# Kernel tuning notes

Hardware: AMD Instinct MI355X
Metric: run time of the kernel (lower is better)

## Reference

```python
import jax, jax.numpy as jnp
import numpy as np

B, S, H = 4, 512, 128

def setup_inputs() -> dict:
    key = jax.random.key(0)
    k_inp, k_m, k_w0, k_b0, k_w1, k_b1 = jax.random.split(key, 6)
    inp = jax.random.normal(k_inp, (B, S, H), dtype=jnp.float32)
    masks = jax.random.randint(k_m, (B, S), 0, 2, dtype=jnp.int32)
    # nn.Linear params: weight [out,in], bias [out]
    lim = 1.0 / np.sqrt(H)
    W0 = jax.random.uniform(k_w0, (H, H), jnp.float32, -lim, lim)
    b0 = jax.random.uniform(k_b0, (H,), jnp.float32, -lim, lim)
    W1 = jax.random.uniform(k_w1, (H, H), jnp.float32, -lim, lim)
    b1 = jax.random.uniform(k_b1, (H,), jnp.float32, -lim, lim)
    return {"inp": inp, "masks": masks, "W0": W0, "b0": b0, "W1": W1, "b1": b1}

def reference(inp, masks, W0, b0, W1, b1):
    # inp: [B,S,H], masks: [B,S] int {0,1}
    mf = masks.astype(inp.dtype)
    sentence_lengths = jnp.sum(mf, axis=1)                      # [B]
    gate_0 = jnp.einsum('bsh,oh->bso', inp, W0) + b0            # [B,S,H]
    gate_1 = jnp.einsum('bsh,oh->bso', inp, W1) + b1            # [B,S,H]
    # pairwise broadcast gate: [B,S(i),S(j),H]
    forget_gate = jax.nn.sigmoid(gate_0[:, :, None, :] + gate_1[:, None, :, :])
    # gate the row-expanded input (inp indexed by j)
    forget_result = inp[:, None, :, :] * forget_gate            # [B,S,S,H]
    pair_mask = mf[:, :, None] * mf[:, None, :]                 # [B,S,S]
    context_sumup = jnp.sum(forget_result * pair_mask[:, :, :, None], axis=2)  # [B,S,H]
    context_vector = context_sumup / sentence_lengths[:, None, None]
    return jnp.tanh(context_vector)
```

## Files before the change

### kernel.cpp

```cpp
#include <hip/hip_runtime.h>
#include <hip/hip_bf16.h>


#define BB 4
#define SS 512
#define HH 128
#define RA 8
#define L2E 1.44269504088896f

__global__ __launch_bounds__(256) void kA(const float* __restrict__ inp,
                                          const int* __restrict__ masks,
                                          const float* __restrict__ W0,
                                          const float* __restrict__ b0,
                                          const float* __restrict__ W1,
                                          const float* __restrict__ b1,
                                          float* __restrict__ E0,
                                          float2* __restrict__ XE,
                                          int* __restrict__ valid_idx,
                                          int* __restrict__ nvalid,
                                          float* __restrict__ rcpL,
                                          float* __restrict__ out) {
    const int bid = blockIdx.x;
    if (bid == 512) {
        int wave = threadIdx.x >> 6, lane = threadIdx.x & 63;
        if (wave >= BB) return;
        int b = wave, base = 0;
        for (int c = 0; c < SS; c += 64) {
            int m = masks[b * SS + c + lane];
            unsigned long long bits = __ballot(m != 0);
            int pos = __popcll(bits & ((1ull << lane) - 1ull));
            if (m) valid_idx[b * SS + base + pos] = c + lane;
            base += __popcll(bits);
        }
        if (lane == 0) {
            nvalid[b] = base;
            rcpL[b] = base ? 1.0f / (float)base : 0.0f;
        }
        return;
    }

    __shared__ float4 sW[32 * 128];

    const int g = bid & 1;
    const int row0 = (bid >> 1) * RA;
    const float* __restrict__ W = g ? W1 : W0;

#pragma unroll
    for (int it = 0; it < 16; ++it) {
        const int flat = it * 256 + threadIdx.x;
        const int q = flat & 31;
        const int o = flat >> 5;
        const float4 w = *(const float4*)(W + (size_t)o * HH + q * 4);
        sW[q * 128 + (o ^ q)] = w;
    }
    __syncthreads();

    const int o = threadIdx.x & 127;
    const int rh = threadIdx.x >> 7;
    const int r0 = row0 + rh * 4;
    const float* __restrict__ xb = inp + (size_t)r0 * HH;
    const float bias = g ? b1[o] : b0[o];

    float acc[4] = {bias, bias, bias, bias};
#pragma unroll 4
    for (int q = 0; q < 32; ++q) {
        const float4 w = sW[q * 128 + (o ^ q)];
#pragma unroll
        for (int r = 0; r < 4; ++r) {
            const float4 x = *(const float4*)(xb + (size_t)r * HH + q * 4);
            float a = acc[r];
            a = fmaf(x.x, w.x, a);
            a = fmaf(x.y, w.y, a);
            a = fmaf(x.z, w.z, a);
            a = fmaf(x.w, w.w, a);
            acc[r] = a;
        }
    }

    if (g == 0) {
#pragma unroll
        for (int r = 0; r < 4; ++r)
            E0[(size_t)(r0 + r) * HH + o] = __builtin_amdgcn_exp2f(acc[r] * L2E);
#pragma unroll
        for (int r = 0; r < 4; ++r)
            if (masks[r0 + r] == 0) out[(size_t)(r0 + r) * HH + o] = 0.0f;
    } else {
#pragma unroll
        for (int r = 0; r < 4; ++r) {
            const float re1 = __builtin_amdgcn_exp2f(-acc[r] * L2E);
            const float x = inp[(size_t)(r0 + r) * HH + o];
            XE[(size_t)(r0 + r) * HH + o] = make_float2(x, re1);
        }
    }
}

__global__ __launch_bounds__(1024) void kB(const float* __restrict__ E0,
                                           const float2* __restrict__ XE,
                                           const int* __restrict__ valid_idx,
                                           const int* __restrict__ nvalid,
                                           const float* __restrict__ rcpL,
                                           float* __restrict__ out) {
    const int b = blockIdx.x >> 7;
    const int qi = blockIdx.x & 127;
    const int nv = nvalid[b];
    const int p0 = qi * 4;
    if (p0 >= nv) return;

    __shared__ float red[8][4][HH];
    __shared__ int s_vj[SS];

    const int tid = threadIdx.x;
    const int h = tid & 127;
    const int oc = tid >> 7;

    if (tid < nv) s_vj[tid] = valid_idx[b * SS + tid];
    __syncthreads();

    const size_t boff = (size_t)b * SS * HH;
    const float* __restrict__ E0b = E0 + boff;
    const float2* __restrict__ XEb = XE + boff;

    float e0r[4];
#pragma unroll
    for (int r = 0; r < 4; ++r)
        e0r[r] = (p0 + r < nv) ? E0b[(size_t)s_vj[p0 + r] * HH + h] : 0.0f;

    const int chunk = (nv + 7) >> 3;
    const int jb = oc * chunk;
    const int je = min(nv, jb + chunk);

    float acc[4] = {0.f, 0.f, 0.f, 0.f};
    float sumx = 0.f;
#pragma unroll 8
    for (int t = jb; t < je; ++t) {
        const int j = s_vj[t];
        const float2 v = XEb[(size_t)j * HH + h];
        const float x = v.x, re1 = v.y;
        sumx += x;
        const float xr = x * re1;
#pragma unroll
        for (int r = 0; r < 4; ++r)
            acc[r] = fmaf(xr, __builtin_amdgcn_rcpf(re1 + e0r[r]), acc[r]);
    }

#pragma unroll
    for (int r = 0; r < 4; ++r) red[oc][r][h] = sumx - acc[r];
    __syncthreads();

    if (tid < 512) {
        const int r = tid >> 7;
        if (p0 + r < nv) {
            const int hh = tid & 127;
            float s = 0.f;
#pragma unroll
            for (int q = 0; q < 8; ++q) s += red[q][r][hh];
            float x = s * rcpL[b];
            x = fminf(fmaxf(x, -30.0f), 30.0f);
            const float e = __builtin_amdgcn_exp2f(x * 2.885390081777927f);
            const float th = (e - 1.0f) * __builtin_amdgcn_rcpf(e + 1.0f);
            out[boff + (size_t)s_vj[p0 + r] * HH + hh] = th;
        }
    }
}

extern "C" void kernel_launch(void* const* d_in, const int* in_sizes, int n_in,
                              void* d_out, int out_size, void* d_ws, size_t ws_size,
                              hipStream_t stream) {
    const float* inp = (const float*)d_in[0];
    const int* masks = (const int*)d_in[1];
    const float* W0 = (const float*)d_in[2];
    const float* b0 = (const float*)d_in[3];
    const float* W1 = (const float*)d_in[4];
    const float* b1 = (const float*)d_in[5];
    float* out = (float*)d_out;

    const size_t nBSH = (size_t)BB * SS * HH;
    float* E0 = (float*)d_ws;
    float2* XE = (float2*)(E0 + nBSH);
    int* valid_idx = (int*)(XE + nBSH);
    int* nvalid = valid_idx + BB * SS;
    float* rcpL = (float*)(nvalid + BB);

    kA<<<513, 256, 0, stream>>>(inp, masks, W0, b0, W1, b1,
                                E0, XE, valid_idx, nvalid, rcpL, out);
    kB<<<BB * (SS / 4), 1024, 0, stream>>>(E0, XE, valid_idx, nvalid, rcpL, out);
}
```

Before: 30.64 us.

## Retile gate GEMM over output-column groups and reformulate sigmoid sum

The projection kernel now has each block own 8 output columns for 128 rows. It stages 32-row input tiles in padded shared memory and keeps a small weight slice resident, instead of loading the full weight matrix per block and reading inputs from global memory. The pairwise kernel computes x*t/(1+t) with t=e0*e1 directly, replacing the sumx minus x/(1+e0/e1) form. This drops the running sum and the subtraction but adds one multiply per term. The GEMM change trades full-weight smem staging for more, smaller input tile loads and extra barriers.

```diff
diff --git a/kernel.cpp b/kernel.cpp
--- a/kernel.cpp
+++ b/kernel.cpp
@@ -5,7 +5,6 @@
 #define BB 4
 #define SS 512
 #define HH 128
-#define RA 8
 #define L2E 1.44269504088896f
 
 __global__ __launch_bounds__(256) void kA(const float* __restrict__ inp,
@@ -39,57 +38,57 @@
         return;
     }
 
-    __shared__ float4 sW[32 * 128];
+    __shared__ float s_x[32][132];
+    __shared__ float4 sW4[8][33];
 
     const int g = bid & 1;
-    const int row0 = (bid >> 1) * RA;
-    const float* __restrict__ W = g ? W1 : W0;
+    const int o0 = ((bid >> 1) & 15) * 8;
+    const int rbase = (bid >> 5) * 128;
+    const int tid = threadIdx.x;
+
+    {
+        const int k4 = tid & 31, ol = tid >> 5;
+        const float* __restrict__ W = g ? W1 : W0;
+        sW4[ol][k4] = *(const float4*)(W + (size_t)(o0 + ol) * HH + k4 * 4);
+    }
+
+    const int o_l = tid & 7;
+    const int rr = tid >> 3;
+    const float bias = (g ? b1 : b0)[o0 + o_l];
 
 #pragma unroll
-    for (int it = 0; it < 16; ++it) {
-        const int flat = it * 256 + threadIdx.x;
-        const int q = flat & 31;
-        const int o = flat >> 5;
-        const float4 w = *(const float4*)(W + (size_t)o * HH + q * 4);
-        sW[q * 128 + (o ^ q)] = w;
-    }
-    __syncthreads();
+    for (int tile = 0; tile < 4; ++tile) {
+        const int rb = rbase + tile * 32;
+        __syncthreads();
+#pragma unroll
+        for (int i = 0; i < 4; ++i) {
+            const int f = i * 256 + tid;
+            const int k4 = f & 31, r = f >> 5;
+            *(float4*)&s_x[r][k4 * 4] =
+                *(const float4*)(inp + (size_t)(rb + r) * HH + k4 * 4);
+        }
+        __syncthreads();
 
-    const int o = threadIdx.x & 127;
-    const int rh = threadIdx.x >> 7;
-    const int r0 = row0 + rh * 4;
-    const float* __restrict__ xb = inp + (size_t)r0 * HH;
-    const float bias = g ? b1[o] : b0[o];
-
-    float acc[4] = {bias, bias, bias, bias};
-#pragma unroll 4
-    for (int q = 0; q < 32; ++q) {
-        const float4 w = sW[q * 128 + (o ^ q)];
-#pragma unroll
-        for (int r = 0; r < 4; ++r) {
-            const float4 x = *(const float4*)(xb + (size_t)r * HH + q * 4);
-            float a = acc[r];
-            a = fmaf(x.x, w.x, a);
-            a = fmaf(x.y, w.y, a);
-            a = fmaf(x.z, w.z, a);
-            a = fmaf(x.w, w.w, a);
-            acc[r] = a;
+        float4 a4 = make_float4(0.f, 0.f, 0.f, 0.f);
+#pragma unroll 8
+        for (int k4 = 0; k4 < 32; ++k4) {
+            const float4 w = sW4[o_l][k4];
+            const float4 x = *(const float4*)&s_x[rr][k4 * 4];
+            a4.x = fmaf(x.x, w.x, a4.x);
+            a4.y = fmaf(x.y, w.y, a4.y);
+            a4.z = fmaf(x.z, w.z, a4.z);
+            a4.w = fmaf(x.w, w.w, a4.w);
         }
-    }
-
-    if (g == 0) {
-#pragma unroll
-        for (int r = 0; r < 4; ++r)
-            E0[(size_t)(r0 + r) * HH + o] = __builtin_amdgcn_exp2f(acc[r] * L2E);
-#pragma unroll
-        for (int r = 0; r < 4; ++r)
-            if (masks[r0 + r] == 0) out[(size_t)(r0 + r) * HH + o] = 0.0f;
-    } else {
-#pragma unroll
-        for (int r = 0; r < 4; ++r) {
-            const float re1 = __builtin_amdgcn_exp2f(-acc[r] * L2E);
-            const float x = inp[(size_t)(r0 + r) * HH + o];
-            XE[(size_t)(r0 + r) * HH + o] = make_float2(x, re1);
+        const float acc = bias + ((a4.x + a4.y) + (a4.z + a4.w));
+        const int grow = rb + rr;
+        const size_t idx = (size_t)grow * HH + o0 + o_l;
+        if (g == 0) {
+            E0[idx] = __builtin_amdgcn_exp2f(acc * L2E);
+            if (masks[grow] == 0) out[idx] = 0.0f;
+        } else {
+            const float e1 = __builtin_amdgcn_exp2f(acc * L2E);
+            const float x = s_x[rr][o0 + o_l];
+            XE[idx] = make_float2(x, e1);
         }
     }
 }
@@ -130,21 +129,20 @@
     const int je = min(nv, jb + chunk);
 
     float acc[4] = {0.f, 0.f, 0.f, 0.f};
-    float sumx = 0.f;
 #pragma unroll 8
     for (int t = jb; t < je; ++t) {
         const int j = s_vj[t];
         const float2 v = XEb[(size_t)j * HH + h];
-        const float x = v.x, re1 = v.y;
-        sumx += x;
-        const float xr = x * re1;
+        const float x = v.x, e1 = v.y;
 #pragma unroll
-        for (int r = 0; r < 4; ++r)
-            acc[r] = fmaf(xr, __builtin_amdgcn_rcpf(re1 + e0r[r]), acc[r]);
+        for (int r = 0; r < 4; ++r) {
+            const float t0 = e0r[r] * e1;
+            acc[r] = fmaf(x * t0, __builtin_amdgcn_rcpf(1.0f + t0), acc[r]);
+        }
     }
 
 #pragma unroll
-    for (int r = 0; r < 4; ++r) red[oc][r][h] = sumx - acc[r];
+    for (int r = 0; r < 4; ++r) red[oc][r][h] = acc[r];
     __syncthreads();
 
     if (tid < 512) {
```

Measured after the change: 30.33 us. About the same (-1.0%).
